# Kernel tuning notes

Hardware: AMD Instinct MI355X
Metric: run time of the kernel (lower is better)

Reference implementation:

```python
import jax, jax.numpy as jnp
import numpy as np

DIM = 1024
NUM_HEADS = 16
HEAD_DIM = DIM // NUM_HEADS
TGT_LEN = 4096


def setup_inputs() -> dict:
    key = jax.random.key(0)
    k1, k2, k3 = jax.random.split(key, 3)
    x = jax.random.normal(k1, (TGT_LEN, DIM), dtype=jnp.float32)
    W_in = jax.random.normal(k2, (3 * DIM, DIM), dtype=jnp.float32) * (DIM ** -0.5)
    W_out = jax.random.normal(k3, (DIM, DIM), dtype=jnp.float32) * (DIM ** -0.5)
    return {"x": x, "W_in": W_in, "W_out": W_out, "tgt_len": TGT_LEN}


def reference(x, W_in, W_out, tgt_len):
    # QKV projection (torch Linear: y = x @ W^T)
    qkv = x @ W_in.T  # [T, 3*dim]
    q, k, v = jnp.split(qkv, 3, axis=-1)
    # [T, dim] -> [H, T, hd]
    q = q.reshape(tgt_len, NUM_HEADS, HEAD_DIM).transpose(1, 0, 2)
    k = k.reshape(tgt_len, NUM_HEADS, HEAD_DIM).transpose(1, 0, 2)
    v = v.reshape(tgt_len, NUM_HEADS, HEAD_DIM).transpose(1, 0, 2)
    scaling = HEAD_DIM ** -0.5
    scores = jnp.einsum('htd,hsd->hts', q, k) * scaling  # [H, T, T]
    # joint softmax over the full (T, T) matrix per head (NOT row-wise)
    maxes = jnp.max(scores, axis=(1, 2), keepdims=True)
    x_exp = jnp.exp(scores - maxes)
    probs = x_exp / jnp.sum(x_exp, axis=(1, 2), keepdims=True)
    attn = jnp.einsum('hts,hsd->htd', probs, v)  # [H, T, hd]
    attn = attn.transpose(1, 0, 2).reshape(tgt_len, DIM)
    return attn @ W_out.T
```

## Files before the change

### kernel.cpp

```cpp
#include <hip/hip_runtime.h>

#define TLEN 4096
#define DIM 1024
#define NHEAD 16
#define HDIM 64
#define QKV_COLS (3 * DIM)
#define QSCALE 0.1803368801111244f
#define NCHUNK 2
#define SCHUNK (TLEN / NCHUNK)
#define TB 256
#define NIT (SCHUNK / 64)

typedef __attribute__((ext_vector_type(8))) short short8;
typedef __attribute__((ext_vector_type(4))) float f32x4;

struct alignas(8) s4 { short v[4]; };

__device__ float g_Lsum[NHEAD];
__device__ float g_recipL[NHEAD];

__global__ void zeroL() {
    if (threadIdx.x < NHEAD) g_Lsum[threadIdx.x] = 0.0f;
}
__global__ void recipL() {
    if (threadIdx.x < NHEAD) g_recipL[threadIdx.x] = 1.0f / g_Lsum[threadIdx.x];
}

__device__ __forceinline__ unsigned bf16_rtne_bits(float x) {
    unsigned u = __float_as_uint(x);
    return (u + 0x7fffu + ((u >> 16) & 1u)) >> 16;
}

__device__ __forceinline__ void cp16(const short* g, short* l) {
    __builtin_amdgcn_global_load_lds(
        (const __attribute__((address_space(1))) unsigned int*)g,
        (__attribute__((address_space(3))) unsigned int*)l,
        16, 0, 0);
}

__device__ __forceinline__ short8 mk8(unsigned a, unsigned b, unsigned c, unsigned d) {
    union { unsigned u[4]; short8 s; } t;
    t.u[0] = a; t.u[1] = b; t.u[2] = c; t.u[3] = d;
    return t.s;
}

__global__ __launch_bounds__(256) void conv_bf16(
    const float* __restrict__ src, short* __restrict__ dst, int n4)
{
    int i = blockIdx.x * 256 + threadIdx.x;
    if (i < n4) {
        float4 v = ((const float4*)src)[i];
        s4 o;
        o.v[0] = (short)bf16_rtne_bits(v.x);
        o.v[1] = (short)bf16_rtne_bits(v.y);
        o.v[2] = (short)bf16_rtne_bits(v.z);
        o.v[3] = (short)bf16_rtne_bits(v.w);
        ((s4*)dst)[i] = o;
    }
}

__global__ __launch_bounds__(256) void conv_wout(
    const float* __restrict__ src, short* __restrict__ dst)
{
    int i = blockIdx.x * 256 + threadIdx.x;
    float s = g_recipL[(i & 255) >> 4];
    float4 v = ((const float4*)src)[i];
    s4 o;
    o.v[0] = (short)bf16_rtne_bits(v.x * s);
    o.v[1] = (short)bf16_rtne_bits(v.y * s);
    o.v[2] = (short)bf16_rtne_bits(v.z * s);
    o.v[3] = (short)bf16_rtne_bits(v.w * s);
    ((s4*)dst)[i] = o;
}

__global__ __launch_bounds__(256) void combine(
    const short* __restrict__ p0, const short* __restrict__ p1,
    short* __restrict__ dst, int n4)
{
    int i = blockIdx.x * 256 + threadIdx.x;
    if (i < n4) {
        s4 a = ((const s4*)p0)[i];
        s4 b = ((const s4*)p1)[i];
        s4 o;
#pragma unroll
        for (int m = 0; m < 4; ++m) {
            float fa = __uint_as_float(((unsigned)(unsigned short)a.v[m]) << 16);
            float fb = __uint_as_float(((unsigned)(unsigned short)b.v[m]) << 16);
            o.v[m] = (short)bf16_rtne_bits(fa + fb);
        }
        ((s4*)dst)[i] = o;
    }
}

template <bool QKV_MODE>
__global__ __launch_bounds__(256) void gemm_bt(
    const short* __restrict__ A, const short* __restrict__ B,
    void* __restrict__ Cout, short* __restrict__ Vout, int M, int N, int K)
{
    __shared__ __align__(16) short As[128][32];
    __shared__ __align__(16) short Bs[128][32];
    const int tid  = threadIdx.x;
    const int wv   = tid >> 6, lane = tid & 63;
    const int fr   = lane & 15, quad = lane >> 4;
    const int wm   = (wv >> 1) * 64, wn = (wv & 1) * 64;
    const int m0 = blockIdx.x * 128, n0 = blockIdx.y * 128;

    f32x4 acc[4][4] = {};

    for (int k0 = 0; k0 < K; k0 += 32) {
        __syncthreads();
#pragma unroll
        for (int c = tid; c < 512; c += 256) {
            int row = c >> 2, col = (c & 3) * 8;
            cp16(A + (size_t)(m0 + row) * K + k0 + col, &As[row][col]);
            cp16(B + (size_t)(n0 + row) * K + k0 + col, &Bs[row][col]);
        }
        __syncthreads();

        short8 af[4], bfr[4];
#pragma unroll
        for (int i = 0; i < 4; ++i) {
            af[i]  = *(const short8*)&As[wm + i * 16 + fr][quad * 8];
            bfr[i] = *(const short8*)&Bs[wn + i * 16 + fr][quad * 8];
        }
#pragma unroll
        for (int i = 0; i < 4; ++i)
#pragma unroll
            for (int j = 0; j < 4; ++j)
                acc[i][j] = __builtin_amdgcn_mfma_f32_16x16x32_bf16(af[i], bfr[j], acc[i][j], 0, 0, 0);
    }

    if (QKV_MODE && n0 >= 2 * DIM) {
#pragma unroll
        for (int i = 0; i < 4; ++i)
#pragma unroll
            for (int j = 0; j < 4; ++j) {
                int n = n0 - 2 * DIM + wn + j * 16 + fr;
                int m = m0 + wm + i * 16 + quad * 4;
                unsigned u0 = bf16_rtne_bits(acc[i][j][0]);
                unsigned u1 = bf16_rtne_bits(acc[i][j][1]);
                unsigned u2 = bf16_rtne_bits(acc[i][j][2]);
                unsigned u3 = bf16_rtne_bits(acc[i][j][3]);
                uint2 pk;
                pk.x = u0 | (u1 << 16);
                pk.y = u2 | (u3 << 16);
                *(uint2*)(Vout + (size_t)n * TLEN + m) = pk;
            }
    } else if (QKV_MODE) {
        const float sc = (n0 < DIM) ? QSCALE : 1.0f;
#pragma unroll
        for (int i = 0; i < 4; ++i)
#pragma unroll
            for (int j = 0; j < 4; ++j)
#pragma unroll
                for (int r = 0; r < 4; ++r) {
                    size_t off = (size_t)(m0 + wm + i * 16 + quad * 4 + r) * N + n0 + wn + j * 16 + fr;
                    ((short*)Cout)[off] = (short)bf16_rtne_bits(acc[i][j][r] * sc);
                }
    } else {
#pragma unroll
        for (int i = 0; i < 4; ++i)
#pragma unroll
            for (int j = 0; j < 4; ++j)
#pragma unroll
                for (int r = 0; r < 4; ++r) {
                    size_t off = (size_t)(m0 + wm + i * 16 + quad * 4 + r) * N + n0 + wn + j * 16 + fr;
                    ((float*)Cout)[off] = acc[i][j][r];
                }
    }
}

__global__ __launch_bounds__(256, 2) void attn_mfma(
    const short* __restrict__ qkvb, const short* __restrict__ vtb,
    short* __restrict__ part)
{
    __shared__ __align__(16) short Ks[2][64][72];
    __shared__ __align__(16) short Vt[2][64][72];
    __shared__ float red[256];

    const int tid = threadIdx.x;
    const int t0 = blockIdx.x * TB;
    const int h  = blockIdx.y;
    const int chunk = blockIdx.z;
    const int srow = tid >> 2;
    const int sch  = (tid & 3) * 16;
    const int wv   = tid >> 6;
    const int lane = tid & 63;
    const int fr   = lane & 15;
    const int quad = lane >> 4;
    const int tb   = wv * 64;

    short8 qf[4][2];
#pragma unroll
    for (int jt = 0; jt < 4; ++jt) {
        const short* qsrc = qkvb + (size_t)(t0 + tb + jt * 16 + fr) * QKV_COLS + h * HDIM + quad * 8;
        qf[jt][0] = *(const short8*)qsrc;
        qf[jt][1] = *(const short8*)(qsrc + 32);
    }

    short8 ones;
#pragma unroll
    for (int m = 0; m < 8; ++m) ones[m] = (short)0x3F80;

    f32x4 oaccT[4][4] = {};
    f32x4 racc[4] = {};

    const int s_begin = chunk * SCHUNK;
    const short* kbase = qkvb + DIM + h * HDIM + sch;
    const short* vbase = vtb + (size_t)(h * HDIM + srow) * TLEN + sch;

    uint4 kA, kB, vA, vB;
    {
        const short* ks = kbase + (size_t)(s_begin + srow) * QKV_COLS;
        kA = *(const uint4*)ks;  kB = *(const uint4*)(ks + 8);
        const short* vs = vbase + s_begin;
        vA = *(const uint4*)vs;  vB = *(const uint4*)(vs + 8);
    }
    *(uint4*)&Ks[0][srow][sch]     = kA;
    *(uint4*)&Ks[0][srow][sch + 8] = kB;
    *(uint4*)&Vt[0][srow][sch]     = vA;
    *(uint4*)&Vt[0][srow][sch + 8] = vB;
    {
        const short* ks = kbase + (size_t)(s_begin + 64 + srow) * QKV_COLS;
        kA = *(const uint4*)ks;  kB = *(const uint4*)(ks + 8);
        const short* vs = vbase + s_begin + 64;
        vA = *(const uint4*)vs;  vB = *(const uint4*)(vs + 8);
    }
    __syncthreads();

    auto step = [&](short (*KsC)[72], short (*VtC)[72],
                    short (*KsN)[72], short (*VtN)[72], int it) {
        if (it + 1 < NIT) {
            *(uint4*)&KsN[srow][sch]     = kA;
            *(uint4*)&KsN[srow][sch + 8] = kB;
            *(uint4*)&VtN[srow][sch]     = vA;
            *(uint4*)&VtN[srow][sch + 8] = vB;
        }
        if (it + 2 < NIT) {
            const int s0n = s_begin + (it + 2) * 64;
            const short* ks = kbase + (size_t)(s0n + srow) * QKV_COLS;
            kA = *(const uint4*)ks;  kB = *(const uint4*)(ks + 8);
            const short* vs = vbase + s0n;
            vA = *(const uint4*)vs;  vB = *(const uint4*)(vs + 8);
        }

        short8 kf[4][2], vf[4][2];
#pragma unroll
        for (int i = 0; i < 4; ++i) {
            kf[i][0] = *(const short8*)&KsC[i * 16 + fr][quad * 8];
            kf[i][1] = *(const short8*)&KsC[i * 16 + fr][32 + quad * 8];
            vf[i][0] = *(const short8*)&VtC[i * 16 + fr][quad * 8];
            vf[i][1] = *(const short8*)&VtC[i * 16 + fr][32 + quad * 8];
        }

#pragma unroll
        for (int jt = 0; jt < 4; ++jt) {
            unsigned w0[4], w1[4];
#pragma unroll
            for (int i = 0; i < 4; ++i) {
                f32x4 acc = {};
                acc = __builtin_amdgcn_mfma_f32_16x16x32_bf16(kf[i][0], qf[jt][0], acc, 0, 0, 0);
                acc = __builtin_amdgcn_mfma_f32_16x16x32_bf16(kf[i][1], qf[jt][1], acc, 0, 0, 0);
                unsigned u0 = __float_as_uint(__builtin_amdgcn_exp2f(acc[0]));
                unsigned u1 = __float_as_uint(__builtin_amdgcn_exp2f(acc[1]));
                unsigned u2 = __float_as_uint(__builtin_amdgcn_exp2f(acc[2]));
                unsigned u3 = __float_as_uint(__builtin_amdgcn_exp2f(acc[3]));
                w0[i] = __builtin_amdgcn_perm(u1, u0, 0x07060302);
                w1[i] = __builtin_amdgcn_perm(u3, u2, 0x07060302);
            }
            auto A0 = __builtin_amdgcn_permlane32_swap(w0[0], w0[1], false, false);
            auto A2 = __builtin_amdgcn_permlane32_swap(w0[2], w0[3], false, false);
            auto B0 = __builtin_amdgcn_permlane32_swap(w1[0], w1[1], false, false);
            auto B2 = __builtin_amdgcn_permlane32_swap(w1[2], w1[3], false, false);
            auto O0 = __builtin_amdgcn_permlane16_swap(A0[0], A0[1], false, false);
            auto O2 = __builtin_amdgcn_permlane16_swap(A2[0], A2[1], false, false);
            auto P0 = __builtin_amdgcn_permlane16_swap(B0[0], B0[1], false, false);
            auto P2 = __builtin_amdgcn_permlane16_swap(B2[0], B2[1], false, false);
            short8 pb0 = mk8(O0[0], P0[0], O0[1], P0[1]);
            short8 pb1 = mk8(O2[0], P2[0], O2[1], P2[1]);

            __builtin_amdgcn_s_setprio(1);
            racc[jt] = __builtin_amdgcn_mfma_f32_16x16x32_bf16(ones, pb0, racc[jt], 0, 0, 0);
            racc[jt] = __builtin_amdgcn_mfma_f32_16x16x32_bf16(ones, pb1, racc[jt], 0, 0, 0);

#pragma unroll
            for (int jd = 0; jd < 4; ++jd) {
                oaccT[jd][jt] = __builtin_amdgcn_mfma_f32_16x16x32_bf16(vf[jd][0], pb0, oaccT[jd][jt], 0, 0, 0);
                oaccT[jd][jt] = __builtin_amdgcn_mfma_f32_16x16x32_bf16(vf[jd][1], pb1, oaccT[jd][jt], 0, 0, 0);
            }
            __builtin_amdgcn_s_setprio(0);
        }
        __syncthreads();
    };

    for (int it = 0; it < NIT; it += 2) {
        step(Ks[0], Vt[0], Ks[1], Vt[1], it);
        step(Ks[1], Vt[1], Ks[0], Vt[0], it + 1);
    }

    short* pc = part + (size_t)chunk * TLEN * DIM;
#pragma unroll
    for (int jt = 0; jt < 4; ++jt)
#pragma unroll
        for (int jd = 0; jd < 4; ++jd) {
            unsigned u0 = bf16_rtne_bits(oaccT[jd][jt][0]);
            unsigned u1 = bf16_rtne_bits(oaccT[jd][jt][1]);
            unsigned u2 = bf16_rtne_bits(oaccT[jd][jt][2]);
            unsigned u3 = bf16_rtne_bits(oaccT[jd][jt][3]);
            uint2 pk;
            pk.x = u0 | (u1 << 16);
            pk.y = u2 | (u3 << 16);
            *(uint2*)(pc + (size_t)(t0 + tb + jt * 16 + fr) * DIM + h * HDIM + jd * 16 + quad * 4) = pk;
        }

    red[tid] = (racc[0][0] + racc[1][0] + racc[2][0] + racc[3][0]) * 0.25f;
    __syncthreads();
    for (int off = 128; off > 0; off >>= 1) {
        if (tid < off) red[tid] += red[tid + off];
        __syncthreads();
    }
    if (tid == 0) atomicAdd(&g_Lsum[h], red[0]);
}

extern "C" void kernel_launch(void* const* d_in, const int* in_sizes, int n_in,
                              void* d_out, int out_size, void* d_ws, size_t ws_size,
                              hipStream_t stream)
{
    const float* x     = (const float*)d_in[0];
    const float* W_in  = (const float*)d_in[1];
    const float* W_out = (const float*)d_in[2];
    float* out = (float*)d_out;

    char* ws = (char*)d_ws;
    short* xb    = (short*)(ws);
    short* wib   = (short*)(ws + (8u << 20));
    short* wob   = (short*)(ws + (14u << 20));
    short* qkvb  = (short*)(ws + (16u << 20));
    short* vtb   = (short*)(ws + (40u << 20));
    short* part  = (short*)(ws + (48u << 20));
    short* attnb = xb;

    zeroL<<<1, 64, 0, stream>>>();

    conv_bf16<<<(TLEN * DIM / 4 + 255) / 256, 256, 0, stream>>>(x, xb, TLEN * DIM / 4);
    conv_bf16<<<(QKV_COLS * DIM / 4 + 255) / 256, 256, 0, stream>>>(W_in, wib, QKV_COLS * DIM / 4);

    gemm_bt<true><<<dim3(TLEN / 128, QKV_COLS / 128), 256, 0, stream>>>(
        xb, wib, qkvb, vtb, TLEN, QKV_COLS, DIM);

    attn_mfma<<<dim3(TLEN / TB, NHEAD, NCHUNK), 256, 0, stream>>>(qkvb, vtb, part);

    recipL<<<1, 64, 0, stream>>>();
    conv_wout<<<(DIM * DIM / 4 + 255) / 256, 256, 0, stream>>>(W_out, wob);

    combine<<<(TLEN * DIM / 4 + 255) / 256, 256, 0, stream>>>(
        part, part + (size_t)TLEN * DIM, attnb, TLEN * DIM / 4);

    gemm_bt<false><<<dim3(TLEN / 128, DIM / 128), 256, 0, stream>>>(
        attnb, wob, out, nullptr, TLEN, DIM, DIM);
}
```

Before: 221.4 us.

## Software-pipeline QK, exp and PV stages with sched_group_barrier interleaving

Splits the per-tile inner loop into separate QK matmul, exp/pack, and PV matmul stages, then software-pipelines them across the four jt tiles with double-buffered score registers. Explicit sched_group_barrier hints interleave MFMA and VALU instructions so exp/permute work overlaps matrix ops. It also drops the s_setprio toggling. The cost is higher register pressure, which could lower occupancy or cause spills.

```diff
diff --git a/kernel.cpp b/kernel.cpp
--- a/kernel.cpp
+++ b/kernel.cpp
@@ -253,18 +253,23 @@
             vf[i][1] = *(const short8*)&VtC[i * 16 + fr][32 + quad * 8];
         }
 
-#pragma unroll
-        for (int jt = 0; jt < 4; ++jt) {
+        auto QK = [&](int jt, f32x4 (&sc)[4]) {
+#pragma unroll
+            for (int i = 0; i < 4; ++i) {
+                f32x4 a = {};
+                a = __builtin_amdgcn_mfma_f32_16x16x32_bf16(kf[i][0], qf[jt][0], a, 0, 0, 0);
+                a = __builtin_amdgcn_mfma_f32_16x16x32_bf16(kf[i][1], qf[jt][1], a, 0, 0, 0);
+                sc[i] = a;
+            }
+        };
+        auto EXP = [&](const f32x4 (&sc)[4], short8 &pb0, short8 &pb1) {
             unsigned w0[4], w1[4];
 #pragma unroll
             for (int i = 0; i < 4; ++i) {
-                f32x4 acc = {};
-                acc = __builtin_amdgcn_mfma_f32_16x16x32_bf16(kf[i][0], qf[jt][0], acc, 0, 0, 0);
-                acc = __builtin_amdgcn_mfma_f32_16x16x32_bf16(kf[i][1], qf[jt][1], acc, 0, 0, 0);
-                unsigned u0 = __float_as_uint(__builtin_amdgcn_exp2f(acc[0]));
-                unsigned u1 = __float_as_uint(__builtin_amdgcn_exp2f(acc[1]));
-                unsigned u2 = __float_as_uint(__builtin_amdgcn_exp2f(acc[2]));
-                unsigned u3 = __float_as_uint(__builtin_amdgcn_exp2f(acc[3]));
+                unsigned u0 = __float_as_uint(__builtin_amdgcn_exp2f(sc[i][0]));
+                unsigned u1 = __float_as_uint(__builtin_amdgcn_exp2f(sc[i][1]));
+                unsigned u2 = __float_as_uint(__builtin_amdgcn_exp2f(sc[i][2]));
+                unsigned u3 = __float_as_uint(__builtin_amdgcn_exp2f(sc[i][3]));
                 w0[i] = __builtin_amdgcn_perm(u1, u0, 0x07060302);
                 w1[i] = __builtin_amdgcn_perm(u3, u2, 0x07060302);
             }
@@ -276,20 +281,55 @@
             auto O2 = __builtin_amdgcn_permlane16_swap(A2[0], A2[1], false, false);
             auto P0 = __builtin_amdgcn_permlane16_swap(B0[0], B0[1], false, false);
             auto P2 = __builtin_amdgcn_permlane16_swap(B2[0], B2[1], false, false);
-            short8 pb0 = mk8(O0[0], P0[0], O0[1], P0[1]);
-            short8 pb1 = mk8(O2[0], P2[0], O2[1], P2[1]);
-
-            __builtin_amdgcn_s_setprio(1);
+            pb0 = mk8(O0[0], P0[0], O0[1], P0[1]);
+            pb1 = mk8(O2[0], P2[0], O2[1], P2[1]);
+        };
+        auto PV = [&](int jt, short8 pb0, short8 pb1) {
             racc[jt] = __builtin_amdgcn_mfma_f32_16x16x32_bf16(ones, pb0, racc[jt], 0, 0, 0);
             racc[jt] = __builtin_amdgcn_mfma_f32_16x16x32_bf16(ones, pb1, racc[jt], 0, 0, 0);
-
 #pragma unroll
             for (int jd = 0; jd < 4; ++jd) {
                 oaccT[jd][jt] = __builtin_amdgcn_mfma_f32_16x16x32_bf16(vf[jd][0], pb0, oaccT[jd][jt], 0, 0, 0);
                 oaccT[jd][jt] = __builtin_amdgcn_mfma_f32_16x16x32_bf16(vf[jd][1], pb1, oaccT[jd][jt], 0, 0, 0);
             }
-            __builtin_amdgcn_s_setprio(0);
-        }
+        };
+
+        f32x4 scA[4], scB[4];
+        short8 pbA0, pbA1, pbB0, pbB1;
+
+        QK(0, scA);
+        QK(1, scB);
+        EXP(scA, pbA0, pbA1);
+#pragma unroll
+        for (int g = 0; g < 8; ++g) {
+            __builtin_amdgcn_sched_group_barrier(0x8, 1, 0);
+            __builtin_amdgcn_sched_group_barrier(0x2, 5, 0);
+        }
+        QK(2, scA);
+        PV(0, pbA0, pbA1);
+        EXP(scB, pbB0, pbB1);
+#pragma unroll
+        for (int g = 0; g < 18; ++g) {
+            __builtin_amdgcn_sched_group_barrier(0x8, 1, 0);
+            __builtin_amdgcn_sched_group_barrier(0x2, 2, 0);
+        }
+        QK(3, scB);
+        PV(1, pbB0, pbB1);
+        EXP(scA, pbA0, pbA1);
+#pragma unroll
+        for (int g = 0; g < 18; ++g) {
+            __builtin_amdgcn_sched_group_barrier(0x8, 1, 0);
+            __builtin_amdgcn_sched_group_barrier(0x2, 2, 0);
+        }
+        PV(2, pbA0, pbA1);
+        EXP(scB, pbB0, pbB1);
+#pragma unroll
+        for (int g = 0; g < 10; ++g) {
+            __builtin_amdgcn_sched_group_barrier(0x8, 1, 0);
+            __builtin_amdgcn_sched_group_barrier(0x2, 4, 0);
+        }
+        PV(3, pbB0, pbB1);
+
         __syncthreads();
     };
 
```

Result: no change. 222.2 us (+0.4%).
